# Kernel optimization log

Hardware: AMD Instinct MI355X
Metric: run time of the kernel (lower is better)

Reference implementation:

```python
import jax, jax.numpy as jnp
import numpy as np

THR = 1.0  # snntorch Leaky default threshold

# Heaviside spike with ATan surrogate gradient (snntorch surrogate.atan, alpha=2)
@jax.custom_vjp
def atan_spike(x):
    return (x > 0).astype(x.dtype)

def _spike_fwd(x):
    return atan_spike(x), x

def _spike_bwd(x, g):
    # d/dx of surrogate: (alpha/2) / (1 + (pi/2*alpha*x)^2) with alpha=2 -> 1/(1+(pi*x)^2)
    return (g / (1.0 + (jnp.pi * x) ** 2),)

atan_spike.defvjp(_spike_fwd, _spike_bwd)


def setup_inputs() -> dict:
    key = jax.random.key(0)
    ks = jax.random.split(key, 5)
    B, T = 256, 100
    D, H, O = 34 * 34 * 2, 1000, 10
    data = jax.random.normal(ks[0], (B, T, 2, 34, 34), jnp.float32)
    lim1 = 1.0 / np.sqrt(D)
    lim2 = 1.0 / np.sqrt(H)
    w1 = jax.random.uniform(ks[1], (H, D), jnp.float32, -lim1, lim1)
    b1 = jax.random.uniform(ks[2], (H,), jnp.float32, -lim1, lim1)
    w2 = jax.random.uniform(ks[3], (O, H), jnp.float32, -lim2, lim2)
    b2 = jax.random.uniform(ks[4], (O,), jnp.float32, -lim2, lim2)
    beta = jnp.float32(0.9)
    return {"data": data, "w1": w1, "b1": b1, "w2": w2, "b2": b2, "beta": beta}


def reference(data, w1, b1, w2, b2, beta):
    B, T = data.shape[0], data.shape[1]
    H, O = w1.shape[0], w2.shape[0]
    x = data.reshape(B, T, -1).transpose(1, 0, 2)  # [T, B, D] (Flatten per step)
    # Input currents to layer 1 are state-independent: one batched GEMM.
    cur1_all = jnp.einsum('tbd,hd->tbh', x, w1) + b1  # [T, B, H]

    mem1 = jnp.zeros((B, H), data.dtype)
    spk1 = jnp.zeros((B, H), data.dtype)
    mem2 = jnp.zeros((B, O), data.dtype)
    spk2 = jnp.zeros((B, O), data.dtype)

    def step(carry, cur1):
        mem1, spk1, mem2, spk2 = carry
        # snntorch Leaky, reset_mechanism='subtract':
        # mem = beta*mem + input - reset*threshold ; spk = fire(mem)
        mem1 = beta * mem1 + cur1 - spk1 * THR
        spk1 = atan_spike(mem1 - THR)
        cur2 = spk1 @ w2.T + b2
        mem2 = beta * mem2 + cur2 - spk2 * THR
        spk2 = atan_spike(mem2 - THR)
        return (mem1, spk1, mem2, spk2), (spk2, mem2)

    _, (spk_rec, mem_rec) = jax.lax.scan(step, (mem1, spk1, mem2, spk2), cur1_all)
    return spk_rec, mem_rec  # each [T, B, 10]
```

## Files before the change

### kernel.cpp

```cpp
#include <hip/hip_runtime.h>
#include <hip/hip_bf16.h>
#include <stdint.h>

#define T_STEPS 100
#define B_SZ    256
#define D_IN    2312
#define H_SZ    1000
#define O_SZ    10
#define M_ROWS  (B_SZ * T_STEPS)
#define K_PAD   2336
#define KT      73
#define W_ROWS  1024

#define A_SCALE   16.0f
#define W_SCALE   64.0f
#define INV_SCALE (1.0f / 1024.0f)

typedef __attribute__((ext_vector_type(4))) float     floatx4;
typedef __attribute__((ext_vector_type(8))) _Float16  halfx8;

#define ASYNC_COPY16(g, l)                                             \
  __builtin_amdgcn_global_load_lds(                                    \
      (const __attribute__((address_space(1))) void*)(g),              \
      (__attribute__((address_space(3))) void*)(l), 16, 0, 0)

__global__ __launch_bounds__(256)
void splitW_kernel(const float* __restrict__ W,
                   _Float16* __restrict__ wHi,
                   _Float16* __restrict__ wLo)
{
  const int r = blockIdx.x;
  const bool rvalid = (r < H_SZ);
  const float* w = W + (size_t)(rvalid ? r : 0) * D_IN;
  _Float16* ho = wHi + (size_t)r * K_PAD;
  _Float16* lo = wLo + (size_t)r * K_PAD;
  for (int c = threadIdx.x; c < K_PAD / 8; c += 256) {
    const int k0 = c * 8;
    const bool v = rvalid && (k0 + 8 <= D_IN);
    _Float16 h[8], l[8];
    #pragma unroll
    for (int e = 0; e < 8; ++e) {
      const float x = v ? w[k0 + e] * W_SCALE : 0.f;
      const _Float16 hb = (_Float16)x;
      h[e] = hb;
      l[e] = (_Float16)(x - (float)hb);
    }
    *reinterpret_cast<uint4*>(ho + k0) = *reinterpret_cast<const uint4*>(h);
    *reinterpret_cast<uint4*>(lo + k0) = *reinterpret_cast<const uint4*>(l);
  }
}

__global__ __launch_bounds__(256)
void gemm1_fused(const float* __restrict__ A,
                 const _Float16* __restrict__ wHi,
                 const _Float16* __restrict__ wLo,
                 const float* __restrict__ b1,
                 float* __restrict__ C)
{
  __shared__ _Float16 sAh[2][128 * 32];
  __shared__ _Float16 sAl[2][128 * 32];
  __shared__ _Float16 sBh[2][128 * 32];
  __shared__ _Float16 sBl[2][128 * 32];

  const int tid  = threadIdx.x;

  const int id  = blockIdx.x;
  const int j   = id >> 3;
  const int mt  = (id & 7) * 25 + (j >> 3);
  const int nt  = j & 7;
  const int m0  = mt * 128;
  const int n0  = nt * 128;

  const int wid  = tid >> 6;
  const int lane = tid & 63;
  const int wm   = (wid & 1) * 64;
  const int wn   = (wid >> 1) * 64;
  const int quad = lane >> 4;
  const int l16  = lane & 15;

  floatx4 acc[4][4];
  #pragma unroll
  for (int i = 0; i < 4; ++i)
    #pragma unroll
    for (int jj = 0; jj < 4; ++jj)
      acc[i][jj] = floatx4{0.f, 0.f, 0.f, 0.f};

  const int r0  = tid >> 2;
  const int r1  = r0 + 64;
  const int sl  = tid & 3;
  const int rho = (r0 >> 1) & 3;
  const int ko  = ((sl ^ rho) * 8);

  const float* gA0 = A + (size_t)(m0 + r0) * D_IN + ko;
  const float* gA1 = A + (size_t)(m0 + r1) * D_IN + ko;
  const _Float16* gBh0 = wHi + (size_t)(n0 + r0) * K_PAD + ko;
  const _Float16* gBh1 = wHi + (size_t)(n0 + r1) * K_PAD + ko;
  const _Float16* gBl0 = wLo + (size_t)(n0 + r0) * K_PAD + ko;
  const _Float16* gBl1 = wLo + (size_t)(n0 + r1) * K_PAD + ko;

  const int la0 = tid * 8;
  const int la1 = (tid + 256) * 8;

  const int fo = (quad ^ ((l16 >> 1) & 3)) * 8;

  float a0[8], a1[8];
  *reinterpret_cast<float4*>(a0)     = *reinterpret_cast<const float4*>(gA0);
  *reinterpret_cast<float4*>(a0 + 4) = *reinterpret_cast<const float4*>(gA0 + 4);
  *reinterpret_cast<float4*>(a1)     = *reinterpret_cast<const float4*>(gA1);
  *reinterpret_cast<float4*>(a1 + 4) = *reinterpret_cast<const float4*>(gA1 + 4);

  ASYNC_COPY16(gBh0, &sBh[0][la0]);
  ASYNC_COPY16(gBh1, &sBh[0][la1]);
  ASYNC_COPY16(gBl0, &sBl[0][la0]);
  ASYNC_COPY16(gBl1, &sBl[0][la1]);

  {
    _Float16 h0[8], l0[8], h1[8], l1[8];
    #pragma unroll
    for (int e = 0; e < 8; ++e) {
      const float v0 = a0[e] * A_SCALE;
      const _Float16 hb0 = (_Float16)v0;
      h0[e] = hb0; l0[e] = (_Float16)(v0 - (float)hb0);
      const float v1 = a1[e] * A_SCALE;
      const _Float16 hb1 = (_Float16)v1;
      h1[e] = hb1; l1[e] = (_Float16)(v1 - (float)hb1);
    }
    *reinterpret_cast<uint4*>(&sAh[0][la0]) = *reinterpret_cast<const uint4*>(h0);
    *reinterpret_cast<uint4*>(&sAl[0][la0]) = *reinterpret_cast<const uint4*>(l0);
    *reinterpret_cast<uint4*>(&sAh[0][la1]) = *reinterpret_cast<const uint4*>(h1);
    *reinterpret_cast<uint4*>(&sAl[0][la1]) = *reinterpret_cast<const uint4*>(l1);
  }

  *reinterpret_cast<float4*>(a0)     = *reinterpret_cast<const float4*>(gA0 + 32);
  *reinterpret_cast<float4*>(a0 + 4) = *reinterpret_cast<const float4*>(gA0 + 36);
  *reinterpret_cast<float4*>(a1)     = *reinterpret_cast<const float4*>(gA1 + 32);
  *reinterpret_cast<float4*>(a1 + 4) = *reinterpret_cast<const float4*>(gA1 + 36);
  bool curValid = true;

  for (int kt = 0; kt < KT; ++kt) {
    const int p = kt & 1;

    __syncthreads();

    halfx8 ah[4], bh[4], al[4], bl[4];
    #pragma unroll
    for (int i = 0; i < 4; ++i) {
      const int row = (wm + i * 16 + l16) * 32 + fo;
      ah[i] = *reinterpret_cast<const halfx8*>(&sAh[p][row]);
      al[i] = *reinterpret_cast<const halfx8*>(&sAl[p][row]);
    }
    #pragma unroll
    for (int jj = 0; jj < 4; ++jj) {
      const int row = (wn + jj * 16 + l16) * 32 + fo;
      bh[jj] = *reinterpret_cast<const halfx8*>(&sBh[p][row]);
      bl[jj] = *reinterpret_cast<const halfx8*>(&sBl[p][row]);
    }

    if (kt + 1 < KT) {
      _Float16 h0[8], l0[8], h1[8], l1[8];
      #pragma unroll
      for (int e = 0; e < 8; ++e) {
        const float v0 = curValid ? a0[e] * A_SCALE : 0.f;
        const _Float16 hb0 = (_Float16)v0;
        h0[e] = hb0; l0[e] = (_Float16)(v0 - (float)hb0);
        const float v1 = curValid ? a1[e] * A_SCALE : 0.f;
        const _Float16 hb1 = (_Float16)v1;
        h1[e] = hb1; l1[e] = (_Float16)(v1 - (float)hb1);
      }
      const int q = p ^ 1;
      *reinterpret_cast<uint4*>(&sAh[q][la0]) = *reinterpret_cast<const uint4*>(h0);
      *reinterpret_cast<uint4*>(&sAl[q][la0]) = *reinterpret_cast<const uint4*>(l0);
      *reinterpret_cast<uint4*>(&sAh[q][la1]) = *reinterpret_cast<const uint4*>(h1);
      *reinterpret_cast<uint4*>(&sAl[q][la1]) = *reinterpret_cast<const uint4*>(l1);

      const int kb = (kt + 1) * 32;
      ASYNC_COPY16(gBh0 + kb, &sBh[q][la0]);
      ASYNC_COPY16(gBh1 + kb, &sBh[q][la1]);
      ASYNC_COPY16(gBl0 + kb, &sBl[q][la0]);
      ASYNC_COPY16(gBl1 + kb, &sBl[q][la1]);
    }

    if (kt + 2 < KT) {
      const int kb2 = (kt + 2) * 32;
      const bool v = (kb2 + ko) < D_IN;
      const int off = v ? kb2 : 0;
      *reinterpret_cast<float4*>(a0)     = *reinterpret_cast<const float4*>(gA0 + off);
      *reinterpret_cast<float4*>(a0 + 4) = *reinterpret_cast<const float4*>(gA0 + off + 4);
      *reinterpret_cast<float4*>(a1)     = *reinterpret_cast<const float4*>(gA1 + off);
      *reinterpret_cast<float4*>(a1 + 4) = *reinterpret_cast<const float4*>(gA1 + off + 4);
      curValid = v;
    }

    #pragma unroll
    for (int i = 0; i < 4; ++i)
      #pragma unroll
      for (int jj = 0; jj < 4; ++jj)
        acc[i][jj] = __builtin_amdgcn_mfma_f32_16x16x32_f16(ah[i], bh[jj], acc[i][jj], 0, 0, 0);
    #pragma unroll
    for (int i = 0; i < 4; ++i)
      #pragma unroll
      for (int jj = 0; jj < 4; ++jj)
        acc[i][jj] = __builtin_amdgcn_mfma_f32_16x16x32_f16(al[i], bh[jj], acc[i][jj], 0, 0, 0);
    #pragma unroll
    for (int i = 0; i < 4; ++i)
      #pragma unroll
      for (int jj = 0; jj < 4; ++jj)
        acc[i][jj] = __builtin_amdgcn_mfma_f32_16x16x32_f16(ah[i], bl[jj], acc[i][jj], 0, 0, 0);
  }

  #pragma unroll
  for (int jj = 0; jj < 4; ++jj) {
    const int col = n0 + wn + jj * 16 + l16;
    if (col < H_SZ) {
      const float bias = b1[col];
      #pragma unroll
      for (int i = 0; i < 4; ++i) {
        const int row = m0 + wm + i * 16 + quad * 4;
        #pragma unroll
        for (int r = 0; r < 4; ++r)
          C[(size_t)(row + r) * H_SZ + col] = acc[i][jj][r] * INV_SCALE + bias;
      }
    }
  }
}

__global__ __launch_bounds__(256)
void scan1_kernel(const float* __restrict__ cur1,
                  const float* __restrict__ beta_p,
                  __hip_bfloat16* __restrict__ spk1)
{
  const int h = blockIdx.x * 256 + threadIdx.x;
  const int b = blockIdx.y;
  if (h >= H_SZ) return;
  const float beta = beta_p[0];
  const float* c    = cur1 + (size_t)b * T_STEPS * H_SZ + h;
  __hip_bfloat16* s = spk1 + (size_t)b * T_STEPS * H_SZ + h;
  float mem = 0.f, spk = 0.f;
  #pragma unroll 4
  for (int t = 0; t < T_STEPS; ++t) {
    mem = beta * mem + c[(size_t)t * H_SZ] - spk;
    spk = (mem > 1.0f) ? 1.0f : 0.0f;
    s[(size_t)t * H_SZ] = __float2bfloat16(spk);
  }
}

__global__ __launch_bounds__(256)
void gemm2_kernel(const __hip_bfloat16* __restrict__ spk1,
                  const float* __restrict__ w2,
                  float* __restrict__ cur2)
{
  const int wid  = threadIdx.x >> 6;
  const int lane = threadIdx.x & 63;
  const int m    = blockIdx.x * 4 + wid;

  float acc[O_SZ];
  #pragma unroll
  for (int o = 0; o < O_SZ; ++o) acc[o] = 0.f;

  const __hip_bfloat16* row = spk1 + (size_t)m * H_SZ;
  #pragma unroll
  for (int it = 0; it < 16; ++it) {
    const int h = it * 64 + lane;
    if (h < H_SZ) {
      const float s = __bfloat162float(row[h]);
      if (s != 0.f) {
        #pragma unroll
        for (int o = 0; o < O_SZ; ++o)
          acc[o] += w2[o * H_SZ + h];
      }
    }
  }
  #pragma unroll
  for (int o = 0; o < O_SZ; ++o) {
    float v = acc[o];
    #pragma unroll
    for (int off = 32; off > 0; off >>= 1) v += __shfl_down(v, off);
    if (lane == 0) cur2[(size_t)m * O_SZ + o] = v;
  }
}

__global__ __launch_bounds__(256)
void scan2_kernel(const float* __restrict__ cur2,
                  const float* __restrict__ b2,
                  const float* __restrict__ beta_p,
                  float* __restrict__ out)
{
  const int idx = blockIdx.x * 256 + threadIdx.x;
  if (idx >= B_SZ * O_SZ) return;
  const int b = idx / O_SZ;
  const int o = idx % O_SZ;
  const float beta = beta_p[0];
  const float bias = b2[o];
  float* spk_rec = out;
  float* mem_rec = out + (size_t)T_STEPS * B_SZ * O_SZ;
  float mem = 0.f, spk = 0.f;
  for (int t = 0; t < T_STEPS; ++t) {
    const float cur = cur2[((size_t)b * T_STEPS + t) * O_SZ + o] + bias;
    mem = beta * mem + cur - spk;
    spk = (mem > 1.0f) ? 1.0f : 0.0f;
    const size_t oi = ((size_t)t * B_SZ + b) * O_SZ + o;
    spk_rec[oi] = spk;
    mem_rec[oi] = mem;
  }
}

extern "C" void kernel_launch(void* const* d_in, const int* in_sizes, int n_in,
                              void* d_out, int out_size, void* d_ws, size_t ws_size,
                              hipStream_t stream)
{
  const float* data = (const float*)d_in[0];
  const float* w1   = (const float*)d_in[1];
  const float* b1   = (const float*)d_in[2];
  const float* w2   = (const float*)d_in[3];
  const float* b2   = (const float*)d_in[4];
  const float* beta = (const float*)d_in[5];
  float* out = (float*)d_out;

  char* p = (char*)d_ws;
  auto take = [&](size_t n) { char* q = p; p += (n + 255) & ~(size_t)255; return q; };
  _Float16*       wHi  = (_Float16*)take((size_t)W_ROWS * K_PAD * 2);
  _Float16*       wLo  = (_Float16*)take((size_t)W_ROWS * K_PAD * 2);
  float*          cur1 = (float*)take((size_t)M_ROWS * H_SZ * 4);
  __hip_bfloat16* spk1 = (__hip_bfloat16*)take((size_t)M_ROWS * H_SZ * 2);
  float*          cur2 = (float*)take((size_t)M_ROWS * O_SZ * 4);

  splitW_kernel<<<dim3(W_ROWS), 256, 0, stream>>>(w1, wHi, wLo);
  gemm1_fused<<<dim3(1600), 256, 0, stream>>>(data, wHi, wLo, b1, cur1);
  scan1_kernel<<<dim3(4, B_SZ), 256, 0, stream>>>(cur1, beta, spk1);
  gemm2_kernel<<<dim3(M_ROWS / 4), 256, 0, stream>>>(spk1, w2, cur2);
  scan2_kernel<<<dim3(10), 256, 0, stream>>>(cur2, b2, beta, out);
}
```

Baseline: 821.0 us.

## Fuse LIF layer-1 scan with GEMM2 and tune GEMM1 barrier scheduling

The layer-1 LIF scan and the spike-by-W2 product are merged into one kernel, with one block per batch element. Each block keeps W2 in registers and reduces the 10 outputs per timestep through wave shuffles and shared memory. This drops the bf16 spike buffer write and its re-read. In GEMM1 the plain __syncthreads is replaced by an explicit waitcnt, vmcnt(4), plus s_barrier, with MFMA sections raised in priority and the two prefetch branches merged. The fused kernel launches only 256 blocks with two syncs per timestep, so it may be latency-bound, and the partial vmcnt wait assumes a particular count of in-flight loads.

```diff
diff --git a/kernel.cpp b/kernel.cpp
--- a/kernel.cpp
+++ b/kernel.cpp
@@ -140,7 +140,10 @@
   for (int kt = 0; kt < KT; ++kt) {
     const int p = kt & 1;
 
-    __syncthreads();
+    asm volatile("s_waitcnt vmcnt(4) lgkmcnt(0)" ::: "memory");
+    __builtin_amdgcn_sched_barrier(0);
+    __builtin_amdgcn_s_barrier();
+    __builtin_amdgcn_sched_barrier(0);
 
     halfx8 ah[4], bh[4], al[4], bl[4];
     #pragma unroll
@@ -178,9 +181,7 @@
       ASYNC_COPY16(gBh1 + kb, &sBh[q][la1]);
       ASYNC_COPY16(gBl0 + kb, &sBl[q][la0]);
       ASYNC_COPY16(gBl1 + kb, &sBl[q][la1]);
-    }
-
-    if (kt + 2 < KT) {
+
       const int kb2 = (kt + 2) * 32;
       const bool v = (kb2 + ko) < D_IN;
       const int off = v ? kb2 : 0;
@@ -191,6 +192,7 @@
       curValid = v;
     }
 
+    __builtin_amdgcn_s_setprio(1);
     #pragma unroll
     for (int i = 0; i < 4; ++i)
       #pragma unroll
@@ -206,6 +208,7 @@
       #pragma unroll
       for (int jj = 0; jj < 4; ++jj)
         acc[i][jj] = __builtin_amdgcn_mfma_f32_16x16x32_f16(ah[i], bl[jj], acc[i][jj], 0, 0, 0);
+    __builtin_amdgcn_s_setprio(0);
   }
 
   #pragma unroll
@@ -225,57 +228,71 @@
 }
 
 __global__ __launch_bounds__(256)
-void scan1_kernel(const float* __restrict__ cur1,
-                  const float* __restrict__ beta_p,
-                  __hip_bfloat16* __restrict__ spk1)
-{
-  const int h = blockIdx.x * 256 + threadIdx.x;
-  const int b = blockIdx.y;
-  if (h >= H_SZ) return;
+void lif1_gemm2_kernel(const float* __restrict__ cur1,
+                       const float* __restrict__ w2,
+                       const float* __restrict__ beta_p,
+                       float* __restrict__ cur2)
+{
+  __shared__ float sRed[4][O_SZ];
+
+  const int tid = threadIdx.x;
+  const int b   = blockIdx.x;
   const float beta = beta_p[0];
-  const float* c    = cur1 + (size_t)b * T_STEPS * H_SZ + h;
-  __hip_bfloat16* s = spk1 + (size_t)b * T_STEPS * H_SZ + h;
-  float mem = 0.f, spk = 0.f;
-  #pragma unroll 4
+
+  float w2r[4][O_SZ];
+  #pragma unroll
+  for (int e = 0; e < 4; ++e) {
+    const int h = tid + 256 * e;
+    #pragma unroll
+    for (int o = 0; o < O_SZ; ++o)
+      w2r[e][o] = (h < H_SZ) ? w2[o * H_SZ + h] : 0.f;
+  }
+
+  const float* c = cur1 + (size_t)b * T_STEPS * H_SZ;
+
+  float mem[4] = {0.f, 0.f, 0.f, 0.f};
+  float spk[4] = {0.f, 0.f, 0.f, 0.f};
+
+  float nxt[4];
+  #pragma unroll
+  for (int e = 0; e < 4; ++e) {
+    const int h = tid + 256 * e;
+    nxt[e] = (h < H_SZ) ? c[h] : 0.f;
+  }
+
   for (int t = 0; t < T_STEPS; ++t) {
-    mem = beta * mem + c[(size_t)t * H_SZ] - spk;
-    spk = (mem > 1.0f) ? 1.0f : 0.0f;
-    s[(size_t)t * H_SZ] = __float2bfloat16(spk);
-  }
-}
-
-__global__ __launch_bounds__(256)
-void gemm2_kernel(const __hip_bfloat16* __restrict__ spk1,
-                  const float* __restrict__ w2,
-                  float* __restrict__ cur2)
-{
-  const int wid  = threadIdx.x >> 6;
-  const int lane = threadIdx.x & 63;
-  const int m    = blockIdx.x * 4 + wid;
-
-  float acc[O_SZ];
-  #pragma unroll
-  for (int o = 0; o < O_SZ; ++o) acc[o] = 0.f;
-
-  const __hip_bfloat16* row = spk1 + (size_t)m * H_SZ;
-  #pragma unroll
-  for (int it = 0; it < 16; ++it) {
-    const int h = it * 64 + lane;
-    if (h < H_SZ) {
-      const float s = __bfloat162float(row[h]);
-      if (s != 0.f) {
-        #pragma unroll
-        for (int o = 0; o < O_SZ; ++o)
-          acc[o] += w2[o * H_SZ + h];
+    float cu[4];
+    #pragma unroll
+    for (int e = 0; e < 4; ++e) cu[e] = nxt[e];
+
+    if (t + 1 < T_STEPS) {
+      const float* cn = c + (size_t)(t + 1) * H_SZ;
+      #pragma unroll
+      for (int e = 0; e < 4; ++e) {
+        const int h = tid + 256 * e;
+        nxt[e] = (h < H_SZ) ? cn[h] : 0.f;
       }
     }
-  }
-  #pragma unroll
-  for (int o = 0; o < O_SZ; ++o) {
-    float v = acc[o];
-    #pragma unroll
-    for (int off = 32; off > 0; off >>= 1) v += __shfl_down(v, off);
-    if (lane == 0) cur2[(size_t)m * O_SZ + o] = v;
+
+    #pragma unroll
+    for (int e = 0; e < 4; ++e) {
+      mem[e] = beta * mem[e] + cu[e] - spk[e];
+      spk[e] = (mem[e] > 1.0f) ? 1.0f : 0.0f;
+    }
+
+    #pragma unroll
+    for (int o = 0; o < O_SZ; ++o) {
+      float v = spk[0] * w2r[0][o] + spk[1] * w2r[1][o]
+              + spk[2] * w2r[2][o] + spk[3] * w2r[3][o];
+      #pragma unroll
+      for (int off = 32; off > 0; off >>= 1) v += __shfl_down(v, off);
+      if ((tid & 63) == 0) sRed[tid >> 6][o] = v;
+    }
+    __syncthreads();
+    if (tid < O_SZ)
+      cur2[((size_t)b * T_STEPS + t) * O_SZ + tid] =
+          sRed[0][tid] + sRed[1][tid] + sRed[2][tid] + sRed[3][tid];
+    __syncthreads();
   }
 }
 
@@ -318,15 +335,13 @@
 
   char* p = (char*)d_ws;
   auto take = [&](size_t n) { char* q = p; p += (n + 255) & ~(size_t)255; return q; };
-  _Float16*       wHi  = (_Float16*)take((size_t)W_ROWS * K_PAD * 2);
-  _Float16*       wLo  = (_Float16*)take((size_t)W_ROWS * K_PAD * 2);
-  float*          cur1 = (float*)take((size_t)M_ROWS * H_SZ * 4);
-  __hip_bfloat16* spk1 = (__hip_bfloat16*)take((size_t)M_ROWS * H_SZ * 2);
-  float*          cur2 = (float*)take((size_t)M_ROWS * O_SZ * 4);
+  _Float16* wHi  = (_Float16*)take((size_t)W_ROWS * K_PAD * 2);
+  _Float16* wLo  = (_Float16*)take((size_t)W_ROWS * K_PAD * 2);
+  float*    cur1 = (float*)take((size_t)M_ROWS * H_SZ * 4);
+  float*    cur2 = (float*)take((size_t)M_ROWS * O_SZ * 4);
 
   splitW_kernel<<<dim3(W_ROWS), 256, 0, stream>>>(w1, wHi, wLo);
   gemm1_fused<<<dim3(1600), 256, 0, stream>>>(data, wHi, wLo, b1, cur1);
-  scan1_kernel<<<dim3(4, B_SZ), 256, 0, stream>>>(cur1, beta, spk1);
-  gemm2_kernel<<<dim3(M_ROWS / 4), 256, 0, stream>>>(spk1, w2, cur2);
+  lif1_gemm2_kernel<<<dim3(B_SZ), 256, 0, stream>>>(cur1, w2, beta, cur2);
   scan2_kernel<<<dim3(10), 256, 0, stream>>>(cur2, b2, beta, out);
 }
```

Measured after the change: 943.5 us. +14.9%, slower.

## Enlarge GEMM1 tile to 256x256 with 8 waves and interleaved split-fp16 MFMAs

Applied to the files above, without the earlier changes.

The layer-1 GEMM now uses 512-thread blocks computing 256x256 output tiles instead of 256-thread blocks on 128x128 tiles. This doubles operand reuse per shared-memory fill and cuts global traffic for the split hi/lo fp16 operands. The full __syncthreads is replaced by an explicit waitcnt plus s_barrier, and MFMA issue is raised in priority with s_setprio. The three hi/lo products are interleaved per accumulator, and A fragments are loaded just before use. In exchange the kernel needs 128 KB of LDS, more accumulator registers and only 400 blocks, which gives poor wave balance across the CUs.

```diff
diff --git a/kernel.cpp b/kernel.cpp
--- a/kernel.cpp
+++ b/kernel.cpp
@@ -50,43 +50,43 @@
   }
 }
 
-__global__ __launch_bounds__(256)
+__global__ __launch_bounds__(512, 2)
 void gemm1_fused(const float* __restrict__ A,
                  const _Float16* __restrict__ wHi,
                  const _Float16* __restrict__ wLo,
                  const float* __restrict__ b1,
                  float* __restrict__ C)
 {
-  __shared__ _Float16 sAh[2][128 * 32];
-  __shared__ _Float16 sAl[2][128 * 32];
-  __shared__ _Float16 sBh[2][128 * 32];
-  __shared__ _Float16 sBl[2][128 * 32];
+  __shared__ _Float16 sAh[2][256 * 32];
+  __shared__ _Float16 sAl[2][256 * 32];
+  __shared__ _Float16 sBh[2][256 * 32];
+  __shared__ _Float16 sBl[2][256 * 32];
 
   const int tid  = threadIdx.x;
 
-  const int id  = blockIdx.x;
-  const int j   = id >> 3;
-  const int mt  = (id & 7) * 25 + (j >> 3);
-  const int nt  = j & 7;
-  const int m0  = mt * 128;
-  const int n0  = nt * 128;
+  const int id = blockIdx.x;
+  const int l  = (id & 7) * 50 + (id >> 3);
+  const int mt = l >> 2;
+  const int nt = l & 3;
+  const int m0 = mt * 256;
+  const int n0 = nt * 256;
 
   const int wid  = tid >> 6;
   const int lane = tid & 63;
-  const int wm   = (wid & 1) * 64;
+  const int wm   = (wid & 1) * 128;
   const int wn   = (wid >> 1) * 64;
   const int quad = lane >> 4;
   const int l16  = lane & 15;
 
-  floatx4 acc[4][4];
-  #pragma unroll
-  for (int i = 0; i < 4; ++i)
+  floatx4 acc[8][4];
+  #pragma unroll
+  for (int i = 0; i < 8; ++i)
     #pragma unroll
     for (int jj = 0; jj < 4; ++jj)
       acc[i][jj] = floatx4{0.f, 0.f, 0.f, 0.f};
 
   const int r0  = tid >> 2;
-  const int r1  = r0 + 64;
+  const int r1  = r0 + 128;
   const int sl  = tid & 3;
   const int rho = (r0 >> 1) & 3;
   const int ko  = ((sl ^ rho) * 8);
@@ -99,7 +99,7 @@
   const _Float16* gBl1 = wLo + (size_t)(n0 + r1) * K_PAD + ko;
 
   const int la0 = tid * 8;
-  const int la1 = (tid + 256) * 8;
+  const int la1 = (tid + 512) * 8;
 
   const int fo = (quad ^ ((l16 >> 1) & 3)) * 8;
 
@@ -140,15 +140,12 @@
   for (int kt = 0; kt < KT; ++kt) {
     const int p = kt & 1;
 
-    __syncthreads();
-
-    halfx8 ah[4], bh[4], al[4], bl[4];
-    #pragma unroll
-    for (int i = 0; i < 4; ++i) {
-      const int row = (wm + i * 16 + l16) * 32 + fo;
-      ah[i] = *reinterpret_cast<const halfx8*>(&sAh[p][row]);
-      al[i] = *reinterpret_cast<const halfx8*>(&sAl[p][row]);
-    }
+    asm volatile("s_waitcnt vmcnt(4) lgkmcnt(0)" ::: "memory");
+    __builtin_amdgcn_sched_barrier(0);
+    __builtin_amdgcn_s_barrier();
+    __builtin_amdgcn_sched_barrier(0);
+
+    halfx8 bh[4], bl[4];
     #pragma unroll
     for (int jj = 0; jj < 4; ++jj) {
       const int row = (wn + jj * 16 + l16) * 32 + fo;
@@ -178,9 +175,7 @@
       ASYNC_COPY16(gBh1 + kb, &sBh[q][la1]);
       ASYNC_COPY16(gBl0 + kb, &sBl[q][la0]);
       ASYNC_COPY16(gBl1 + kb, &sBl[q][la1]);
-    }
-
-    if (kt + 2 < KT) {
+
       const int kb2 = (kt + 2) * 32;
       const bool v = (kb2 + ko) < D_IN;
       const int off = v ? kb2 : 0;
@@ -191,21 +186,20 @@
       curValid = v;
     }
 
-    #pragma unroll
-    for (int i = 0; i < 4; ++i)
+    __builtin_amdgcn_s_setprio(1);
+    #pragma unroll
+    for (int i = 0; i < 8; ++i) {
+      const int row = (wm + i * 16 + l16) * 32 + fo;
+      const halfx8 ah = *reinterpret_cast<const halfx8*>(&sAh[p][row]);
+      const halfx8 al = *reinterpret_cast<const halfx8*>(&sAl[p][row]);
       #pragma unroll
-      for (int jj = 0; jj < 4; ++jj)
-        acc[i][jj] = __builtin_amdgcn_mfma_f32_16x16x32_f16(ah[i], bh[jj], acc[i][jj], 0, 0, 0);
-    #pragma unroll
-    for (int i = 0; i < 4; ++i)
-      #pragma unroll
-      for (int jj = 0; jj < 4; ++jj)
-        acc[i][jj] = __builtin_amdgcn_mfma_f32_16x16x32_f16(al[i], bh[jj], acc[i][jj], 0, 0, 0);
-    #pragma unroll
-    for (int i = 0; i < 4; ++i)
-      #pragma unroll
-      for (int jj = 0; jj < 4; ++jj)
-        acc[i][jj] = __builtin_amdgcn_mfma_f32_16x16x32_f16(ah[i], bl[jj], acc[i][jj], 0, 0, 0);
+      for (int jj = 0; jj < 4; ++jj) {
+        acc[i][jj] = __builtin_amdgcn_mfma_f32_16x16x32_f16(ah, bh[jj], acc[i][jj], 0, 0, 0);
+        acc[i][jj] = __builtin_amdgcn_mfma_f32_16x16x32_f16(al, bh[jj], acc[i][jj], 0, 0, 0);
+        acc[i][jj] = __builtin_amdgcn_mfma_f32_16x16x32_f16(ah, bl[jj], acc[i][jj], 0, 0, 0);
+      }
+    }
+    __builtin_amdgcn_s_setprio(0);
   }
 
   #pragma unroll
@@ -214,7 +208,7 @@
     if (col < H_SZ) {
       const float bias = b1[col];
       #pragma unroll
-      for (int i = 0; i < 4; ++i) {
+      for (int i = 0; i < 8; ++i) {
         const int row = m0 + wm + i * 16 + quad * 4;
         #pragma unroll
         for (int r = 0; r < 4; ++r)
@@ -325,7 +319,7 @@
   float*          cur2 = (float*)take((size_t)M_ROWS * O_SZ * 4);
 
   splitW_kernel<<<dim3(W_ROWS), 256, 0, stream>>>(w1, wHi, wLo);
-  gemm1_fused<<<dim3(1600), 256, 0, stream>>>(data, wHi, wLo, b1, cur1);
+  gemm1_fused<<<dim3(400), 512, 0, stream>>>(data, wHi, wLo, b1, cur1);
   scan1_kernel<<<dim3(4, B_SZ), 256, 0, stream>>>(cur1, beta, spk1);
   gemm2_kernel<<<dim3(M_ROWS / 4), 256, 0, stream>>>(spk1, w2, cur2);
   scan2_kernel<<<dim3(10), 256, 0, stream>>>(cur2, b2, beta, out);
```

Result: faster. 763.6 us (-7.0%).
